# Kernel tuning notes

Hardware: AMD Instinct MI355X
Metric: run time of the kernel (lower is better)

## Reference

```python
import jax, jax.numpy as jnp
import numpy as np
from jax.scipy.special import logsumexp

N = 4096
SINKHORN_ITERS = 50
EPS = 1e-9


def setup_inputs() -> dict:
    key = jax.random.key(0)
    # Matrix param init: torch.rand(n, n) * 2 - 1
    matrix = jax.random.uniform(key, (N, N), dtype=jnp.float32) * 2.0 - 1.0
    return {"matrix": matrix}


def reference(matrix):
    # RandomMap.P() with sinkhorn=True: 50 iterations of row then column
    # logsumexp normalization in log space, then exp + clamp_min(1e-9).
    def body(i, log_p):
        log_p = log_p - logsumexp(log_p, axis=1, keepdims=True)  # row normalize
        log_p = log_p - logsumexp(log_p, axis=0, keepdims=True)  # col normalize
        return log_p

    log_p = jax.lax.fori_loop(0, SINKHORN_ITERS, body, matrix)
    return jnp.maximum(jnp.exp(log_p), EPS)
```

## Files before the change

### kernel.cpp

```cpp
#include <hip/hip_runtime.h>
#include <cstdint>
#include <cstddef>

#define NN 4096
#define ITERS 50
#define TB 256
#define TSTRIDE 264
#define NBLK 256
#define NTHR 1024

typedef _Float16 half4v __attribute__((ext_vector_type(4)));
typedef _Float16 half8v __attribute__((ext_vector_type(8)));

#define T_BYTES (TB * TSTRIDE * 2)
#define RED_FLOATS 4096
#define SMEM_BYTES (T_BYTES + RED_FLOATS * 4 + 1024 + 1024)

#define SCOPE __HIP_MEMORY_SCOPE_AGENT


#define CNT_ONE (1ull << 52)
#define VAL_MASK (CNT_ONE - 1ull)

__global__ void sk_zero(unsigned long long* __restrict__ b) {
    size_t i = (size_t)blockIdx.x * blockDim.x + threadIdx.x;
    __hip_atomic_store(&b[i], 0ull, __ATOMIC_RELAXED, SCOPE);
}

__device__ __forceinline__ unsigned long long poll16(const unsigned long long* p) {
    unsigned long long v = __hip_atomic_load(p, __ATOMIC_RELAXED, SCOPE);
    while ((v >> 52) < 16ull) {
        __builtin_amdgcn_s_sleep(1);
        v = __hip_atomic_load(p, __ATOMIC_RELAXED, SCOPE);
    }
    return v;
}

__device__ __forceinline__ float unpack_recip(unsigned long long v) {
    return 1.0f / ((float)(v & VAL_MASK) * 0x1p-32f);
}

__device__ __forceinline__ unsigned long long packp(float s) {
    return CNT_ONE | (unsigned long long)(s * 4294967296.0f);
}

__global__ __launch_bounds__(NTHR) void sk_coop(const float* __restrict__ M,
                                                float* __restrict__ out,
                                                unsigned long long* __restrict__ rbuf,
                                                unsigned long long* __restrict__ cbuf) {
    extern __shared__ char smem[];
    _Float16* T   = (_Float16*)smem;
    float*    red = (float*)(smem + T_BYTES);
    float*    rcv = red + RED_FLOATS;
    float*    rrv = rcv + 256;

    const int t  = threadIdx.x;
    const int bi = blockIdx.x >> 4;
    const int bj = blockIdx.x & 15;
    const float* Mt = M + ((size_t)bi * TB) * NN + (size_t)bj * TB;

    #pragma unroll
    for (int i = 0; i < 16; ++i) {
        int idx = t + i * NTHR;
        int r = idx >> 6, c4 = idx & 63;
        float4 m = *(const float4*)(Mt + (size_t)r * NN + c4 * 4);
        half4v h;
        h[0] = (_Float16)__expf(m.x);
        h[1] = (_Float16)__expf(m.y);
        h[2] = (_Float16)__expf(m.z);
        h[3] = (_Float16)__expf(m.w);
        *(half4v*)&T[r * TSTRIDE + c4 * 4] = h;
    }

    for (int it = 0; it < ITERS; ++it) {
        unsigned long long* rb = rbuf + (size_t)(it & 3) * NN;
        unsigned long long* cb = cbuf + (size_t)(it & 3) * NN;

        if (it == 0) {
            if (t < TB) {
                rcv[t] = 1.0f;
                __hip_atomic_store(&cbuf[(size_t)1 * NN + (size_t)bj * TB + t],
                                   0ull, __ATOMIC_RELAXED, SCOPE);
            }
            __syncthreads();
        } else {
            if (t < TB) {
                unsigned long long v = poll16(
                    &cbuf[(size_t)((it - 1) & 3) * NN + (size_t)bj * TB + t]);
                rcv[t] = unpack_recip(v);
                __hip_atomic_store(&cbuf[(size_t)((it + 1) & 3) * NN
                                         + (size_t)bj * TB + t],
                                   0ull, __ATOMIC_RELAXED, SCOPE);
            }
            __syncthreads();
        }

        {
            const int row = t & 255, q = t >> 8;
            const half8v* Trow = (const half8v*)&T[row * TSTRIDE + q * 64];
            const float4* rc4  = (const float4*)(rcv + q * 64);
            float s = 0.0f;
            #pragma unroll
            for (int k = 0; k < 8; ++k) {
                half8v hv = Trow[k];
                float4 c0 = rc4[2 * k];
                float4 c1 = rc4[2 * k + 1];
                s += (float)hv[0] * c0.x + (float)hv[1] * c0.y +
                     (float)hv[2] * c0.z + (float)hv[3] * c0.w +
                     (float)hv[4] * c1.x + (float)hv[5] * c1.y +
                     (float)hv[6] * c1.z + (float)hv[7] * c1.w;
            }
            red[q * 256 + row] = s;
        }
        __syncthreads();

        if (t < TB) {
            float s = red[t] + red[256 + t] + red[512 + t] + red[768 + t];
            unsigned long long pk = packp(s);
            asm volatile("s_waitcnt vmcnt(0)" ::: "memory");
            unsigned long long* p = &rb[(size_t)bi * TB + t];
            __hip_atomic_fetch_add(p, pk, __ATOMIC_RELAXED, SCOPE);
            unsigned long long v = poll16(p);
            rrv[t] = unpack_recip(v);
            __hip_atomic_store(&rbuf[(size_t)((it + 2) & 3) * NN
                                     + (size_t)bi * TB + t],
                               0ull, __ATOMIC_RELAXED, SCOPE);
        }
        __syncthreads();

        {
            const int ch = t & 31, sub = t >> 5;
            const int w = t >> 6, lane = t & 63;
            float acc[8] = {0, 0, 0, 0, 0, 0, 0, 0};
            #pragma unroll
            for (int r = 0; r < 8; ++r) {
                const int row = sub * 8 + r;
                half8v hv = *(const half8v*)&T[row * TSTRIDE + ch * 8];
                float rr = rrv[row];
                #pragma unroll
                for (int j = 0; j < 8; ++j) acc[j] += (float)hv[j] * rr;
            }
            #pragma unroll
            for (int j = 0; j < 8; ++j) acc[j] += __shfl_down(acc[j], 32);
            if (lane < 32) {
                const int rot = (lane >> 2) & 7;
                float* rd = red + w * 256 + ch * 8;
                #pragma unroll
                for (int jj = 0; jj < 8; ++jj) {
                    int j = (jj + rot) & 7;
                    rd[j] = acc[j];
                }
            }
        }
        __syncthreads();

        if (t < TB) {
            float s = 0.0f;
            #pragma unroll
            for (int w = 0; w < 16; ++w) s += red[w * 256 + t];
            unsigned long long pk = packp(s);
            asm volatile("s_waitcnt vmcnt(0)" ::: "memory");
            __hip_atomic_fetch_add(&cb[(size_t)bj * TB + t], pk,
                                   __ATOMIC_RELAXED, SCOPE);
        }
    }

    if (t < TB) {
        unsigned long long v = poll16(
            &cbuf[(size_t)((ITERS - 1) & 3) * NN + (size_t)bj * TB + t]);
        rcv[t] = unpack_recip(v);
    }
    __syncthreads();

    float* outt = out + ((size_t)bi * TB) * NN + (size_t)bj * TB;
    #pragma unroll
    for (int i = 0; i < 16; ++i) {
        int idx = t + i * NTHR;
        int r = idx >> 6, c4 = idx & 63;
        float4 m = *(const float4*)(Mt + (size_t)r * NN + c4 * 4);
        float rr = rrv[r];
        float4 c = ((const float4*)rcv)[c4];
        float4 o;
        o.x = fmaxf(__expf(m.x) * rr * c.x, 1e-9f);
        o.y = fmaxf(__expf(m.y) * rr * c.y, 1e-9f);
        o.z = fmaxf(__expf(m.z) * rr * c.z, 1e-9f);
        o.w = fmaxf(__expf(m.w) * rr * c.w, 1e-9f);
        *(float4*)(outt + (size_t)r * NN + c4 * 4) = o;
    }
}


__global__ __launch_bounds__(256) void sk_init(float* __restrict__ rc,
                                               float* __restrict__ c_sum) {
    int j = blockIdx.x * 256 + threadIdx.x;
    rc[j] = 1.0f;
    c_sum[j] = 0.0f;
}

__global__ __launch_bounds__(256) void sk_exp(const float* __restrict__ M,
                                              float* __restrict__ E) {
    size_t idx = ((size_t)blockIdx.x * 256 + threadIdx.x) * 4;
    float4 m = *(const float4*)(M + idx);
    float4 e;
    e.x = __expf(m.x); e.y = __expf(m.y); e.z = __expf(m.z); e.w = __expf(m.w);
    *(float4*)(E + idx) = e;
}

template<bool HAS_E>
__global__ __launch_bounds__(256) void sk_row(const float* __restrict__ Mat,
                                              const float* __restrict__ rc,
                                              float* __restrict__ rr) {
    const int wave = threadIdx.x >> 6;
    const int lane = threadIdx.x & 63;
    const int row  = blockIdx.x * 4 + wave;
    const float4* __restrict__ Mrow = (const float4*)(Mat + (size_t)row * NN);
    const float4* __restrict__ RC   = (const float4*)rc;
    float s = 0.0f;
    #pragma unroll 4
    for (int k = lane; k < NN / 4; k += 64) {
        float4 m = Mrow[k];
        float4 c = RC[k];
        if (!HAS_E) {
            m.x = __expf(m.x); m.y = __expf(m.y);
            m.z = __expf(m.z); m.w = __expf(m.w);
        }
        s += m.x * c.x + m.y * c.y + m.z * c.z + m.w * c.w;
    }
    #pragma unroll
    for (int off = 32; off > 0; off >>= 1) s += __shfl_down(s, off, 64);
    if (lane == 0) rr[row] = 1.0f / s;
}

template<bool HAS_E>
__global__ __launch_bounds__(256) void sk_col(const float* __restrict__ Mat,
                                              const float* __restrict__ rr,
                                              float* __restrict__ c_sum) {
    const int j  = blockIdx.x * 256 + threadIdx.x;
    const int r0 = blockIdx.y * 64;
    const float* __restrict__ rrp = rr + r0;
    const float* __restrict__ p   = Mat + (size_t)r0 * NN + j;
    float s = 0.0f;
    #pragma unroll 8
    for (int i = 0; i < 64; ++i) {
        float m = p[(size_t)i * NN];
        if (!HAS_E) m = __expf(m);
        s += m * rrp[i];
    }
    atomicAdd(&c_sum[j], s);
}

__global__ __launch_bounds__(256) void sk_recip(float* __restrict__ c_sum,
                                                float* __restrict__ rc) {
    int j = blockIdx.x * 256 + threadIdx.x;
    rc[j] = 1.0f / c_sum[j];
    c_sum[j] = 0.0f;
}

template<bool HAS_E>
__global__ __launch_bounds__(256) void sk_final(const float* __restrict__ Mat,
                                                const float* __restrict__ rr,
                                                const float* __restrict__ rc,
                                                float* __restrict__ out) {
    const int row = blockIdx.y;
    const int c4  = blockIdx.x * 256 + threadIdx.x;
    float4 m = ((const float4*)(Mat + (size_t)row * NN))[c4];
    if (!HAS_E) {
        m.x = __expf(m.x); m.y = __expf(m.y);
        m.z = __expf(m.z); m.w = __expf(m.w);
    }
    float4 c = ((const float4*)rc)[c4];
    float  r = rr[row];
    float4 o;
    o.x = fmaxf(m.x * r * c.x, 1e-9f);
    o.y = fmaxf(m.y * r * c.y, 1e-9f);
    o.z = fmaxf(m.z * r * c.z, 1e-9f);
    o.w = fmaxf(m.w * r * c.w, 1e-9f);
    ((float4*)out)[(size_t)row * (NN / 4) + c4] = o;
}

static void launch_fallback(const float* M, float* out, char* ws, size_t ws_size,
                            hipStream_t stream) {
    float* rc    = (float*)(ws);
    float* rr    = (float*)(ws + 16 * 1024);
    float* c_sum = (float*)(ws + 32 * 1024);
    float* E     = (float*)(ws + 64 * 1024);

    const size_t need_e = 64 * 1024 + (size_t)NN * NN * sizeof(float);
    const bool   has_e  = ws_size >= need_e;

    sk_init<<<NN / 256, 256, 0, stream>>>(rc, c_sum);

    const float* Mat = M;
    if (has_e) {
        sk_exp<<<(NN * (size_t)NN) / 1024, 256, 0, stream>>>(M, E);
        Mat = E;
    }

    dim3 gcol(16, 64);
    for (int it = 0; it < ITERS; ++it) {
        if (has_e) sk_row<true ><<<NN / 4, 256, 0, stream>>>(Mat, rc, rr);
        else       sk_row<false><<<NN / 4, 256, 0, stream>>>(Mat, rc, rr);
        if (has_e) sk_col<true ><<<gcol, 256, 0, stream>>>(Mat, rr, c_sum);
        else       sk_col<false><<<gcol, 256, 0, stream>>>(Mat, rr, c_sum);
        sk_recip<<<NN / 256, 256, 0, stream>>>(c_sum, rc);
    }

    dim3 gfin(4, NN);
    if (has_e) sk_final<true ><<<gfin, 256, 0, stream>>>(Mat, rr, rc, out);
    else       sk_final<false><<<gfin, 256, 0, stream>>>(Mat, rr, rc, out);
}

extern "C" void kernel_launch(void* const* d_in, const int* in_sizes, int n_in,
                              void* d_out, int out_size, void* d_ws, size_t ws_size,
                              hipStream_t stream) {
    const float* M   = (const float*)d_in[0];
    float*       out = (float*)d_out;
    char*        ws  = (char*)d_ws;

    unsigned long long* rbuf = (unsigned long long*)ws;
    unsigned long long* cbuf = rbuf + 4 * NN;
    const size_t ws_need = (size_t)8 * NN * sizeof(unsigned long long);

    int dev = 0;
    (void)hipGetDevice(&dev);
    int coop = 0;
    (void)hipDeviceGetAttribute(&coop, hipDeviceAttributeCooperativeLaunch, dev);
    hipError_t eattr = hipFuncSetAttribute(
        (const void*)sk_coop, hipFuncAttributeMaxDynamicSharedMemorySize, SMEM_BYTES);

    bool done = false;
    if (coop && eattr == hipSuccess && ws_size >= ws_need) {
        sk_zero<<<16, 512, 0, stream>>>(rbuf);
        void* args[4] = {(void*)&M, (void*)&out, (void*)&rbuf, (void*)&cbuf};
        hipError_t e = hipLaunchCooperativeKernel((void*)sk_coop, dim3(NBLK),
                                                  dim3(NTHR), args, SMEM_BYTES,
                                                  stream);
        done = (e == hipSuccess);
    }
    if (!done) launch_fallback(M, out, ws, ws_size, stream);
}
```

Measured before the change: 605.9 us.

## Replace packed atomic-add counters with per-block partial slots and sign-tag polling

```diff
diff --git a/kernel.cpp b/kernel.cpp
--- a/kernel.cpp
+++ b/kernel.cpp
@@ -8,6 +8,7 @@
 #define TSTRIDE 264
 #define NBLK 256
 #define NTHR 1024
+#define SLOT (16 * NN)
 
 typedef _Float16 half4v __attribute__((ext_vector_type(4)));
 typedef _Float16 half8v __attribute__((ext_vector_type(8)));
@@ -19,35 +20,53 @@
 #define SCOPE __HIP_MEMORY_SCOPE_AGENT
 
 
-#define CNT_ONE (1ull << 52)
-#define VAL_MASK (CNT_ONE - 1ull)
-
-__global__ void sk_zero(unsigned long long* __restrict__ b) {
+__global__ void sk_zero(float* __restrict__ b) {
     size_t i = (size_t)blockIdx.x * blockDim.x + threadIdx.x;
-    __hip_atomic_store(&b[i], 0ull, __ATOMIC_RELAXED, SCOPE);
-}
-
-__device__ __forceinline__ unsigned long long poll16(const unsigned long long* p) {
-    unsigned long long v = __hip_atomic_load(p, __ATOMIC_RELAXED, SCOPE);
-    while ((v >> 52) < 16ull) {
+    __hip_atomic_store(&b[i], 0.0f, __ATOMIC_RELAXED, SCOPE);
+}
+
+__device__ __forceinline__ float pload(const float* p) {
+    return __hip_atomic_load(p, __ATOMIC_RELAXED, SCOPE);
+}
+__device__ __forceinline__ void pstore(float* p, float v) {
+    __hip_atomic_store(p, v, __ATOMIC_RELAXED, SCOPE);
+}
+
+__device__ __forceinline__ float poll_sum16(const float* __restrict__ src,
+                                            int own_g, float own_v, int t,
+                                            bool neg) {
+    float vals[16];
+    #pragma unroll
+    for (int g = 0; g < 16; ++g)
+        vals[g] = (g == own_g) ? own_v : pload(&src[g * 256 + t]);
+    unsigned miss = 0;
+    #pragma unroll
+    for (int g = 0; g < 16; ++g) {
+        bool ok = neg ? (vals[g] < 0.0f) : (vals[g] > 0.0f);
+        if (g != own_g && !ok) miss |= (1u << g);
+    }
+    int guard = 1 << 20;
+    while (miss && --guard) {
         __builtin_amdgcn_s_sleep(1);
-        v = __hip_atomic_load(p, __ATOMIC_RELAXED, SCOPE);
-    }
-    return v;
-}
-
-__device__ __forceinline__ float unpack_recip(unsigned long long v) {
-    return 1.0f / ((float)(v & VAL_MASK) * 0x1p-32f);
-}
-
-__device__ __forceinline__ unsigned long long packp(float s) {
-    return CNT_ONE | (unsigned long long)(s * 4294967296.0f);
+        #pragma unroll
+        for (int g = 0; g < 16; ++g)
+            if (miss & (1u << g)) {
+                float v = pload(&src[g * 256 + t]);
+                vals[g] = v;
+                bool ok = neg ? (v < 0.0f) : (v > 0.0f);
+                if (ok) miss &= ~(1u << g);
+            }
+    }
+    float s = 0.0f;
+    #pragma unroll
+    for (int g = 0; g < 16; ++g) s += fabsf(vals[g]);
+    return s;
 }
 
 __global__ __launch_bounds__(NTHR) void sk_coop(const float* __restrict__ M,
                                                 float* __restrict__ out,
-                                                unsigned long long* __restrict__ rbuf,
-                                                unsigned long long* __restrict__ cbuf) {
+                                                float* __restrict__ rbuf,
+                                                float* __restrict__ cbuf) {
     extern __shared__ char smem[];
     _Float16* T   = (_Float16*)smem;
     float*    red = (float*)(smem + T_BYTES);
@@ -72,28 +91,23 @@
         *(half4v*)&T[r * TSTRIDE + c4 * 4] = h;
     }
 
+    float my_cp = 0.0f;
+
     for (int it = 0; it < ITERS; ++it) {
-        unsigned long long* rb = rbuf + (size_t)(it & 3) * NN;
-        unsigned long long* cb = cbuf + (size_t)(it & 3) * NN;
+        const float tag  = (((unsigned)it >> 1) & 1u) ? -1.0f : 1.0f;
+        const bool  sneg = (((unsigned)it >> 1) & 1u) != 0u;
 
         if (it == 0) {
-            if (t < TB) {
-                rcv[t] = 1.0f;
-                __hip_atomic_store(&cbuf[(size_t)1 * NN + (size_t)bj * TB + t],
-                                   0ull, __ATOMIC_RELAXED, SCOPE);
-            }
-            __syncthreads();
+            if (t < TB) rcv[t] = 1.0f;
         } else {
             if (t < TB) {
-                unsigned long long v = poll16(
-                    &cbuf[(size_t)((it - 1) & 3) * NN + (size_t)bj * TB + t]);
-                rcv[t] = unpack_recip(v);
-                __hip_atomic_store(&cbuf[(size_t)((it + 1) & 3) * NN
-                                         + (size_t)bj * TB + t],
-                                   0ull, __ATOMIC_RELAXED, SCOPE);
-            }
-            __syncthreads();
-        }
+                const bool pneg = (((unsigned)(it - 1) >> 1) & 1u) != 0u;
+                const float* src = cbuf + (size_t)((it - 1) & 1) * SLOT
+                                 + (size_t)bj * (16 * TB);
+                rcv[t] = 1.0f / poll_sum16(src, bi, my_cp, t, pneg);
+            }
+        }
+        __syncthreads();
 
         {
             const int row = t & 255, q = t >> 8;
@@ -116,15 +130,10 @@
 
         if (t < TB) {
             float s = red[t] + red[256 + t] + red[512 + t] + red[768 + t];
-            unsigned long long pk = packp(s);
-            asm volatile("s_waitcnt vmcnt(0)" ::: "memory");
-            unsigned long long* p = &rb[(size_t)bi * TB + t];
-            __hip_atomic_fetch_add(p, pk, __ATOMIC_RELAXED, SCOPE);
-            unsigned long long v = poll16(p);
-            rrv[t] = unpack_recip(v);
-            __hip_atomic_store(&rbuf[(size_t)((it + 2) & 3) * NN
-                                     + (size_t)bi * TB + t],
-                               0ull, __ATOMIC_RELAXED, SCOPE);
+            float* rb = rbuf + (size_t)(it & 1) * SLOT;
+            pstore(&rb[((size_t)bi * 16 + bj) * TB + t], s * tag);
+            rrv[t] = 1.0f / poll_sum16(rb + (size_t)bi * (16 * TB), bj, s, t,
+                                       sneg);
         }
         __syncthreads();
 
@@ -158,17 +167,17 @@
             float s = 0.0f;
             #pragma unroll
             for (int w = 0; w < 16; ++w) s += red[w * 256 + t];
-            unsigned long long pk = packp(s);
-            asm volatile("s_waitcnt vmcnt(0)" ::: "memory");
-            __hip_atomic_fetch_add(&cb[(size_t)bj * TB + t], pk,
-                                   __ATOMIC_RELAXED, SCOPE);
+            my_cp = s;
+            pstore(&cbuf[(size_t)(it & 1) * SLOT
+                         + ((size_t)bj * 16 + bi) * TB + t], s * tag);
         }
     }
 
     if (t < TB) {
-        unsigned long long v = poll16(
-            &cbuf[(size_t)((ITERS - 1) & 3) * NN + (size_t)bj * TB + t]);
-        rcv[t] = unpack_recip(v);
+        const bool pneg = (((unsigned)(ITERS - 1) >> 1) & 1u) != 0u;
+        const float* src = cbuf + (size_t)((ITERS - 1) & 1) * SLOT
+                         + (size_t)bj * (16 * TB);
+        rcv[t] = 1.0f / poll_sum16(src, bi, my_cp, t, pneg);
     }
     __syncthreads();
 
@@ -317,9 +326,9 @@
     float*       out = (float*)d_out;
     char*        ws  = (char*)d_ws;
 
-    unsigned long long* rbuf = (unsigned long long*)ws;
-    unsigned long long* cbuf = rbuf + 4 * NN;
-    const size_t ws_need = (size_t)8 * NN * sizeof(unsigned long long);
+    float* rbuf = (float*)ws;
+    float* cbuf = rbuf + (size_t)2 * SLOT;
+    const size_t ws_need = (size_t)4 * SLOT * sizeof(float);
 
     int dev = 0;
     (void)hipGetDevice(&dev);
@@ -330,7 +339,7 @@
 
     bool done = false;
     if (coop && eattr == hipSuccess && ws_size >= ws_need) {
-        sk_zero<<<16, 512, 0, stream>>>(rbuf);
+        sk_zero<<<256, 1024, 0, stream>>>(rbuf);
         void* args[4] = {(void*)&M, (void*)&out, (void*)&rbuf, (void*)&cbuf};
         hipError_t e = hipLaunchCooperativeKernel((void*)sk_coop, dim3(NBLK),
                                                   dim3(NTHR), args, SMEM_BYTES,
```

New measurement: 612.7 us. About the same (+1.1%).
